# Kernel tuning notes

Hardware: AMD Instinct MI355X
Metric: run time of the kernel (lower is better)

The kernel has to match this reference:

```python
import jax, jax.numpy as jnp
import numpy as np

HEADS, OUT_CH = 8, 32  # GATConv(128, 256//8, heads=8) -> concat width 256
NEG_SLOPE = 0.2


def setup_inputs() -> dict:
    key = jax.random.key(0)
    ks = jax.random.split(key, 12)
    N, E, F_IN = 50000, 500000, 128
    H, C = HEADS, OUT_CH
    HID = H * C            # 256
    x = jax.random.normal(ks[0], (N, F_IN), dtype=jnp.float32)
    edge_index = jax.random.randint(ks[1], (2, E), 0, N, dtype=jnp.int64)
    s = 1.0 / np.sqrt(F_IN)
    W_gat = jax.random.normal(ks[2], (F_IN, H * C), dtype=jnp.float32) * s
    att_src = jax.random.normal(ks[3], (H, C), dtype=jnp.float32) * (1.0 / np.sqrt(C))
    att_dst = jax.random.normal(ks[4], (H, C), dtype=jnp.float32) * (1.0 / np.sqrt(C))
    b_gat = jnp.zeros((HID,), dtype=jnp.float32)
    W1 = jax.random.normal(ks[5], (HID, HID // 2), dtype=jnp.float32) * (1.0 / np.sqrt(HID))
    b1 = jnp.zeros((HID // 2,), dtype=jnp.float32)
    W2 = jax.random.normal(ks[6], (HID // 2, 6), dtype=jnp.float32) * (1.0 / np.sqrt(HID // 2))
    b2 = jnp.zeros((6,), dtype=jnp.float32)
    return {"x": x, "edge_index": edge_index, "W_gat": W_gat, "att_src": att_src,
            "att_dst": att_dst, "b_gat": b_gat, "W1": W1, "b1": b1, "W2": W2, "b2": b2}


def _gat_forward(x, edge_index, W_gat, att_src, att_dst, b_gat):
    N = x.shape[0]
    H, C = HEADS, OUT_CH
    # add self loops (PyG GATConv default)
    loop = jnp.arange(N, dtype=edge_index.dtype)
    src = jnp.concatenate([edge_index[0], loop])
    dst = jnp.concatenate([edge_index[1], loop])
    # per-node transform: [N, H, C]
    xh = (x @ W_gat).reshape(N, H, C)
    a_src = jnp.einsum('nhc,hc->nh', xh, att_src)  # [N, H]
    a_dst = jnp.einsum('nhc,hc->nh', xh, att_dst)  # [N, H]
    alpha = a_src[src] + a_dst[dst]                # [Etot, H]
    alpha = jnp.where(alpha >= 0, alpha, NEG_SLOPE * alpha)  # leaky relu
    # segment softmax over destination nodes
    m = jax.ops.segment_max(alpha, dst, num_segments=N)     # [N, H]
    m = jax.lax.stop_gradient(m)
    ex = jnp.exp(alpha - m[dst])
    denom = jax.ops.segment_sum(ex, dst, num_segments=N)    # [N, H]
    coef = ex / denom[dst]                                   # [Etot, H]
    # weighted scatter-add aggregation
    msgs = xh[src] * coef[:, :, None]                        # [Etot, H, C]
    out = jax.ops.segment_sum(msgs, dst, num_segments=N)     # [N, H, C]
    return out.reshape(N, H * C) + b_gat


def reference(x, edge_index, W_gat, att_src, att_dst, b_gat, W1, b1, W2, b2):
    h = _gat_forward(x, edge_index, W_gat, att_src, att_dst, b_gat)
    h = jax.nn.elu(h)
    g = jnp.mean(h, axis=0, keepdims=True)   # [1, 256] mean pool
    g = jax.nn.relu(g @ W1 + b1)
    return g @ W2 + b2                        # [1, 6] logits
```

## Files before the change

### kernel.cpp

```cpp
#include <hip/hip_runtime.h>
#include <hip/hip_fp8.h>
#include <math.h>

#define F_IN 128
#define HID 256
#define NH 8
#define CAP 40
#define BCAP 4096
#define AGG_BLOCKS 768

typedef _Float16 h16;
typedef __attribute__((ext_vector_type(8))) _Float16 half8;
typedef __attribute__((ext_vector_type(4))) float f32x4;

__device__ inline unsigned char f32_to_fp8(float v) {
#if __has_builtin(__builtin_amdgcn_cvt_pk_fp8_f32)
    return (unsigned char)(__builtin_amdgcn_cvt_pk_fp8_f32(v, v, 0, false) & 0xff);
#else
    __hip_fp8_e4m3 t(v);
    return (unsigned char)t.__x;
#endif
}

__device__ inline void fp8x4_to_f32(int w, float* out) {
#if __has_builtin(__builtin_amdgcn_cvt_pk_f32_fp8)
    auto lo = __builtin_amdgcn_cvt_pk_f32_fp8(w, false);
    auto hi = __builtin_amdgcn_cvt_pk_f32_fp8(w, true);
    out[0] = lo[0]; out[1] = lo[1]; out[2] = hi[0]; out[3] = hi[1];
#else
    #pragma unroll
    for (int k = 0; k < 4; ++k) {
        __hip_fp8_e4m3 t;
        t.__x = (unsigned char)((w >> (8 * k)) & 0xff);
        out[k] = (float)t;
    }
#endif
}

__global__ void k_prep(const float* __restrict__ Wg,
                       const float* __restrict__ att_s,
                       const float* __restrict__ att_d,
                       h16* __restrict__ Wt_sw,
                       int* gcur, float* g2, int n) {
    int i = blockIdx.x * 256 + threadIdx.x;
    if (i < 256) gcur[i] = 0;
    if (i < 256 * HID) g2[i] = 0.f;
    if (i < 4352) {
        int fid = i;
        int lane16 = fid & 15;
        int quad = (fid >> 4) & 3;
        int ks = (fid >> 6) & 3;
        int ct = fid >> 8;
        int k0 = ks * 32 + quad * 8;
        half8 v;
        if (ct < 16) {
            int col = ct * 16 + lane16;
            #pragma unroll
            for (int j = 0; j < 8; ++j) v[j] = (h16)Wg[(size_t)(k0 + j) * HID + col];
        } else {
            const float* att = (lane16 < 8) ? att_s : att_d;
            int h = lane16 & 7;
            #pragma unroll
            for (int j = 0; j < 8; ++j) {
                float s = 0.f;
                for (int c = 0; c < 32; ++c)
                    s += Wg[(size_t)(k0 + j) * HID + h * 32 + c] * att[h * 32 + c];
                v[j] = (h16)s;
            }
        }
        *(half8*)(Wt_sw + (size_t)fid * 8) = v;
    }
}

__global__ __launch_bounds__(512) void k_ga(const float* __restrict__ x,
                                            const h16* __restrict__ Wt_sw,
                                            const int* __restrict__ dstp,
                                            const int* __restrict__ srcp,
                                            unsigned char* __restrict__ xh8,
                                            float* __restrict__ a_src,
                                            float* __restrict__ a_dst,
                                            unsigned int* __restrict__ gbuck,
                                            int* __restrict__ gcur,
                                            int n, int e, int ntiles,
                                            int nbuck, int npart) {
    __shared__ __align__(16) char smem[65536];
    int t = threadIdx.x;

    if (blockIdx.x < (unsigned)npart) {
        int* hist  = (int*)smem;
        int* scn   = hist + 256;
        int* lbase = scn + 256;
        int* lcur  = lbase + 256;
        int* base  = lcur + 256;
        unsigned int* sorted = (unsigned int*)(base + 256);
        int c0 = blockIdx.x * 4096;

        if (t < 256) hist[t] = 0;
        __syncthreads();

        unsigned int w8[8];
        int b8[8];
        #pragma unroll
        for (int k = 0; k < 8; ++k) {
            int i = c0 + k * 512 + t;
            if (i < e) {
                int d = dstp[i];
                int s = srcp[i];
                int b = d >> 8;
                b8[k] = b;
                w8[k] = ((unsigned)b << 24) | ((unsigned)(d & 255) << 16) | (unsigned)s;
                atomicAdd(&hist[b], 1);
            } else {
                b8[k] = -1;
                w8[k] = 0;
            }
        }
        __syncthreads();
        if (t < 256) scn[t] = hist[t];
        __syncthreads();
        for (int off = 1; off < 256; off <<= 1) {
            int u = 0;
            if (t < 256 && t >= off) u = scn[t - off];
            __syncthreads();
            if (t < 256 && t >= off) scn[t] += u;
            __syncthreads();
        }
        if (t < 256) {
            lbase[t] = scn[t] - hist[t];
            lcur[t] = 0;
            if (t < nbuck && hist[t] > 0) base[t] = atomicAdd(&gcur[t], hist[t]);
        }
        __syncthreads();
        #pragma unroll
        for (int k = 0; k < 8; ++k) {
            if (b8[k] >= 0) {
                int r = atomicAdd(&lcur[b8[k]], 1);
                sorted[lbase[b8[k]] + r] = w8[k];
            }
        }
        __syncthreads();
        int total = scn[255];
        for (int j = t; j < total; j += 512) {
            unsigned int w = sorted[j];
            int b = w >> 24;
            int addr = base[b] + (j - lbase[b]);
            if (addr < BCAP) gbuck[(size_t)b * BCAP + addr] = w;
        }
        return;
    }

    h16* wlds = (h16*)smem;
    int w = t >> 6, l = t & 63;
    int lane16 = l & 15, quad = l >> 4;

    float4 pv0[4], pv1[4];
    half8 bA[4];
    int tile = (blockIdx.x - npart) * 8 + w;
    bool have = tile < ntiles;
    int row0 = tile * 16;
    {
        const half8* wq = (const half8*)Wt_sw;
        #pragma unroll
        for (int ks = 0; ks < 4; ++ks) bA[ks] = wq[(64 + ks) * 64 + l];
    }
    if (have) {
        int rA = row0 + lane16;
        if (rA >= n) rA = n - 1;
        const float* xrow = x + (size_t)rA * F_IN + quad * 8;
        #pragma unroll
        for (int ks = 0; ks < 4; ++ks) {
            pv0[ks] = *(const float4*)(xrow + ks * 32);
            pv1[ks] = *(const float4*)(xrow + ks * 32 + 4);
        }
    }
    {
        const int4* wsrc = (const int4*)Wt_sw;
        int4* wdst = (int4*)wlds;
        #pragma unroll
        for (int i = 0; i < 8; ++i) wdst[i * 512 + t] = wsrc[i * 512 + t];
    }
    __syncthreads();
    if (!have) return;
    const h16* wl = wlds + (size_t)l * 8;

    half8 afr[4];
    #pragma unroll
    for (int ks = 0; ks < 4; ++ks) {
        half8 a;
        a[0] = (h16)pv0[ks].x; a[1] = (h16)pv0[ks].y;
        a[2] = (h16)pv0[ks].z; a[3] = (h16)pv0[ks].w;
        a[4] = (h16)pv1[ks].x; a[5] = (h16)pv1[ks].y;
        a[6] = (h16)pv1[ks].z; a[7] = (h16)pv1[ks].w;
        afr[ks] = a;
    }
    f32x4 acc[16];
    #pragma unroll
    for (int ct = 0; ct < 16; ++ct) acc[ct] = (f32x4){0.f, 0.f, 0.f, 0.f};
    #pragma unroll
    for (int ct = 0; ct < 16; ++ct) {
        #pragma unroll
        for (int ks = 0; ks < 4; ++ks) {
            half8 bfr = *(const half8*)(wl + (ct * 4 + ks) * 512);
            acc[ct] = __builtin_amdgcn_mfma_f32_16x16x32_f16(afr[ks], bfr, acc[ct], 0, 0, 0);
        }
    }
    f32x4 acc16 = (f32x4){0.f, 0.f, 0.f, 0.f};
    #pragma unroll
    for (int ks = 0; ks < 4; ++ks)
        acc16 = __builtin_amdgcn_mfma_f32_16x16x32_f16(afr[ks], bA[ks], acc16, 0, 0, 0);

    if (row0 + 16 <= n) {
        #pragma unroll
        for (int ct = 0; ct < 16; ++ct) {
            int col = ct * 16 + lane16;
            #pragma unroll
            for (int r = 0; r < 4; ++r)
                xh8[(size_t)(row0 + quad * 4 + r) * HID + col] = f32_to_fp8(acc[ct][r]);
        }
        float* ap = (lane16 < 8) ? a_src : a_dst;
        int h = lane16 & 7;
        #pragma unroll
        for (int r = 0; r < 4; ++r)
            ap[(row0 + quad * 4 + r) * NH + h] = acc16[r];
    } else {
        #pragma unroll
        for (int ct = 0; ct < 16; ++ct) {
            int col = ct * 16 + lane16;
            #pragma unroll
            for (int r = 0; r < 4; ++r) {
                int row = row0 + quad * 4 + r;
                if (row < n) xh8[(size_t)row * HID + col] = f32_to_fp8(acc[ct][r]);
            }
        }
        float* ap = (lane16 < 8) ? a_src : a_dst;
        int h = lane16 & 7;
        #pragma unroll
        for (int r = 0; r < 4; ++r) {
            int row = row0 + quad * 4 + r;
            if (row < n) ap[row * NH + h] = acc16[r];
        }
    }
}

__global__ __launch_bounds__(256) void k_bin(const unsigned int* __restrict__ gbuck,
                                             const int* __restrict__ gcur,
                                             int* __restrict__ cnt,
                                             unsigned short* __restrict__ bin,
                                             int n, int nbuck) {
    __shared__ int hist[256];
    __shared__ int cur[256];
    __shared__ __align__(16) unsigned short bl[256 * CAP];
    int t = threadIdx.x;
    int b = blockIdx.x;
    int count = gcur[b];
    if (count > BCAP) count = BCAP;
    hist[t] = 0;
    __syncthreads();
    const unsigned int* bb = gbuck + (size_t)b * BCAP;
    for (int j = t; j < count; j += 256) atomicAdd(&hist[(bb[j] >> 16) & 255], 1);
    __syncthreads();
    int node = b * 256 + t;
    if (node < n) {
        int hh = hist[t];
        cnt[node] = hh > CAP ? CAP : hh;
    }
    cur[t] = 0;
    __syncthreads();
    for (int j = t; j < count; j += 256) {
        unsigned int wv = bb[j];
        int dl = (wv >> 16) & 255;
        int pos = atomicAdd(&cur[dl], 1);
        if (pos < CAP) bl[dl * CAP + pos] = (unsigned short)(wv & 0xffff);
    }
    __syncthreads();
    const int4* s4 = (const int4*)bl;
    int4* d4 = (int4*)(bin + (size_t)b * 256 * CAP);
    #pragma unroll
    for (int q = 0; q < 5; ++q) d4[q * 256 + t] = s4[q * 256 + t];
}

__global__ __launch_bounds__(256) void k_agg(const unsigned char* __restrict__ xh8,
                                             const float* __restrict__ a_src,
                                             const float* __restrict__ a_dst,
                                             const int* __restrict__ cnt,
                                             const unsigned short* __restrict__ bin,
                                             const float* __restrict__ b_gat,
                                             float* __restrict__ g2, int n, int ntl) {
    __shared__ float wpart[4][260];
    int t = threadIdx.x;
    int slot = t >> 4;
    int cl = t & 15;
    int c0 = cl * 16;
    int h = cl >> 1;

    float vacc[16];
    #pragma unroll
    for (int i = 0; i < 16; ++i) vacc[i] = 0.f;

    for (int tile = blockIdx.x; tile < ntl; tile += gridDim.x) {
        int nn = tile * 16 + slot;
        bool alive = nn < n;
        int nnc = alive ? nn : (n - 1);

        float ad = a_dst[nnc * NH + h];
        int deg = cnt[nnc];
        if (deg > CAP) deg = CAP;

        float al = a_src[nnc * NH + h] + ad;
        al = al > 0.f ? al : 0.2f * al;
        float ex = __expf(al);
        float den = ex;
        float acc[16];
        {
            int4 v = *(const int4*)(xh8 + (size_t)nnc * HID + c0);
            float f[16];
            fp8x4_to_f32(v.x, f); fp8x4_to_f32(v.y, f + 4);
            fp8x4_to_f32(v.z, f + 8); fp8x4_to_f32(v.w, f + 12);
            #pragma unroll
            for (int i = 0; i < 16; ++i) acc[i] = ex * f[i];
        }
        const unsigned short* brow = bin + (size_t)nnc * CAP;
        int j = 0;
        for (; j + 4 <= deg; j += 4) {
            ushort4 ss = *(const ushort4*)(brow + j);
            int s0 = ss.x, s1 = ss.y, s2 = ss.z, s3 = ss.w;
            float aa[4];
            aa[0] = a_src[s0 * NH + h];
            aa[1] = a_src[s1 * NH + h];
            aa[2] = a_src[s2 * NH + h];
            aa[3] = a_src[s3 * NH + h];
            int4 v0 = *(const int4*)(xh8 + (size_t)s0 * HID + c0);
            int4 v1 = *(const int4*)(xh8 + (size_t)s1 * HID + c0);
            int4 v2 = *(const int4*)(xh8 + (size_t)s2 * HID + c0);
            int4 v3 = *(const int4*)(xh8 + (size_t)s3 * HID + c0);
            float e4[4];
            #pragma unroll
            for (int q = 0; q < 4; ++q) {
                float a2 = aa[q] + ad;
                a2 = a2 > 0.f ? a2 : 0.2f * a2;
                e4[q] = __expf(a2);
                den += e4[q];
            }
            float f[16];
            fp8x4_to_f32(v0.x, f); fp8x4_to_f32(v0.y, f + 4);
            fp8x4_to_f32(v0.z, f + 8); fp8x4_to_f32(v0.w, f + 12);
            #pragma unroll
            for (int i = 0; i < 16; ++i) acc[i] += e4[0] * f[i];
            fp8x4_to_f32(v1.x, f); fp8x4_to_f32(v1.y, f + 4);
            fp8x4_to_f32(v1.z, f + 8); fp8x4_to_f32(v1.w, f + 12);
            #pragma unroll
            for (int i = 0; i < 16; ++i) acc[i] += e4[1] * f[i];
            fp8x4_to_f32(v2.x, f); fp8x4_to_f32(v2.y, f + 4);
            fp8x4_to_f32(v2.z, f + 8); fp8x4_to_f32(v2.w, f + 12);
            #pragma unroll
            for (int i = 0; i < 16; ++i) acc[i] += e4[2] * f[i];
            fp8x4_to_f32(v3.x, f); fp8x4_to_f32(v3.y, f + 4);
            fp8x4_to_f32(v3.z, f + 8); fp8x4_to_f32(v3.w, f + 12);
            #pragma unroll
            for (int i = 0; i < 16; ++i) acc[i] += e4[3] * f[i];
        }
        for (; j < deg; ++j) {
            int s = brow[j];
            float a2 = a_src[s * NH + h] + ad;
            a2 = a2 > 0.f ? a2 : 0.2f * a2;
            float e2 = __expf(a2);
            den += e2;
            int4 v = *(const int4*)(xh8 + (size_t)s * HID + c0);
            float f[16];
            fp8x4_to_f32(v.x, f); fp8x4_to_f32(v.y, f + 4);
            fp8x4_to_f32(v.z, f + 8); fp8x4_to_f32(v.w, f + 12);
            #pragma unroll
            for (int i = 0; i < 16; ++i) acc[i] += e2 * f[i];
        }
        float inv = 1.f / den;
        #pragma unroll
        for (int q = 0; q < 4; ++q) {
            float4 bv = *(const float4*)(b_gat + c0 + q * 4);
            float v0 = acc[q * 4 + 0] * inv + bv.x;
            float v1 = acc[q * 4 + 1] * inv + bv.y;
            float v2 = acc[q * 4 + 2] * inv + bv.z;
            float v3 = acc[q * 4 + 3] * inv + bv.w;
            v0 = v0 > 0.f ? v0 : expm1f(v0);
            v1 = v1 > 0.f ? v1 : expm1f(v1);
            v2 = v2 > 0.f ? v2 : expm1f(v2);
            v3 = v3 > 0.f ? v3 : expm1f(v3);
            if (alive) {
                vacc[q * 4 + 0] += v0;
                vacc[q * 4 + 1] += v1;
                vacc[q * 4 + 2] += v2;
                vacc[q * 4 + 3] += v3;
            }
        }
    }
    #pragma unroll
    for (int i = 0; i < 16; ++i) {
        vacc[i] += __shfl_xor(vacc[i], 16, 64);
        vacc[i] += __shfl_xor(vacc[i], 32, 64);
    }
    int w = t >> 6, lw = t & 63;
    if (lw < 16) {
        #pragma unroll
        for (int q = 0; q < 4; ++q)
            *(f32x4*)(&wpart[w][c0 + q * 4]) =
                (f32x4){vacc[q * 4], vacc[q * 4 + 1], vacc[q * 4 + 2], vacc[q * 4 + 3]};
    }
    __syncthreads();
    float s = wpart[0][t] + wpart[1][t] + wpart[2][t] + wpart[3][t];
    atomicAdd(&g2[(blockIdx.x & 255) * HID + t], s);
}

__global__ __launch_bounds__(256) void k_mlp(const float* __restrict__ g2,
                                             const float* __restrict__ W1,
                                             const float* __restrict__ b1,
                                             const float* __restrict__ W2,
                                             const float* __restrict__ b2,
                                             float* __restrict__ out, int n) {
    __shared__ float gm[HID];
    __shared__ float h1p[2][128];
    __shared__ float h1[128];
    int t = threadIdx.x;
    float s = 0.f;
    for (int b = 0; b < 256; ++b) s += g2[b * HID + t];
    gm[t] = s / (float)n;
    __syncthreads();
    int o = t & 127, hf = t >> 7;
    float a = 0.f;
    #pragma unroll 4
    for (int k = hf * 128; k < hf * 128 + 128; ++k) a += gm[k] * W1[k * 128 + o];
    h1p[hf][o] = a;
    __syncthreads();
    if (t < 128) {
        float v = h1p[0][t] + h1p[1][t] + b1[t];
        h1[t] = v > 0.f ? v : 0.f;
    }
    __syncthreads();
    if (t < 6) {
        float a2 = b2[t];
        for (int k = 0; k < 128; ++k) a2 += h1[k] * W2[k * 6 + t];
        out[t] = a2;
    }
}

extern "C" void kernel_launch(void* const* d_in, const int* in_sizes, int n_in,
                              void* d_out, int out_size, void* d_ws, size_t ws_size,
                              hipStream_t stream) {
    const float* x     = (const float*)d_in[0];
    const int*   ei    = (const int*)d_in[1];
    const float* Wg    = (const float*)d_in[2];
    const float* att_s = (const float*)d_in[3];
    const float* att_d = (const float*)d_in[4];
    const float* b_gat = (const float*)d_in[5];
    const float* W1    = (const float*)d_in[6];
    const float* b1    = (const float*)d_in[7];
    const float* W2    = (const float*)d_in[8];
    const float* b2    = (const float*)d_in[9];

    int N = in_sizes[0] / F_IN;
    int E = in_sizes[1] / 2;
    const int* srcp = ei;
    const int* dstp = ei + E;
    int nblk = (N + 15) / 16;
    int ntiles = (N + 15) / 16;
    int nbuck = (N + 255) >> 8;

    char* ws = (char*)d_ws;
    size_t off = 0;
    auto alloc = [&](size_t bytes) {
        size_t o = off;
        off += (bytes + 255) & ~(size_t)255;
        return o;
    };
    unsigned char* xh8 = (unsigned char*)(ws + alloc((size_t)N * HID));
    h16*   Wt      = (h16*)(ws + alloc((size_t)4352 * 16));
    float* asr     = (float*)(ws + alloc((size_t)N * NH * 4));
    float* ads     = (float*)(ws + alloc((size_t)N * NH * 4));
    int*   cnt     = (int*)(ws + alloc((size_t)N * 4));
    unsigned short* bin = (unsigned short*)(ws + alloc((size_t)nbuck * 256 * CAP * 2));
    float* g2      = (float*)(ws + alloc((size_t)256 * HID * 4));
    unsigned int* gbuck = (unsigned int*)(ws + alloc((size_t)nbuck * BCAP * 4));
    int*   gcur    = (int*)(ws + alloc((size_t)256 * 4));

    int npart = (E + 4095) / 4096;
    int ngemm = (ntiles + 7) / 8;
    int naggb = nblk < AGG_BLOCKS ? nblk : AGG_BLOCKS;

    k_prep<<<256, 256, 0, stream>>>(Wg, att_s, att_d, Wt, gcur, g2, N);
    k_ga<<<npart + ngemm, 512, 0, stream>>>(x, Wt, dstp, srcp,
                                            xh8, asr, ads, gbuck, gcur,
                                            N, E, ntiles, nbuck, npart);
    k_bin<<<nbuck, 256, 0, stream>>>(gbuck, gcur, cnt, bin, N, nbuck);
    k_agg<<<naggb, 256, 0, stream>>>(xh8, asr, ads, cnt, bin, b_gat, g2, N, nblk);
    k_mlp<<<1, 256, 0, stream>>>(g2, W1, b1, W2, b2, (float*)d_out, N);
}
```

Measured before the change: 181.7 us.

## Fuse binning, aggregation and MLP into one kernel with last-block finalize

Merges the bucket-binning, attention aggregation and MLP head into a single kernel. Each block takes a quarter of a bucket, builds its neighbor lists in shared memory, aggregates its 64 nodes, then the last block to finish (tracked by an atomic counter) runs the MLP. This removes two kernel launches and the global cnt/bin round trip, and shrinks the partial-sum buffer. The cost is that each bucket's edge list is scanned four times, and the grid is fixed at about 4 blocks per bucket instead of a persistent grid.

After: 233.3 us. 1.28x slower.

```diff
diff --git a/kernel.cpp b/kernel.cpp
--- a/kernel.cpp
+++ b/kernel.cpp
@@ -7,7 +7,7 @@
 #define NH 8
 #define CAP 40
 #define BCAP 4096
-#define AGG_BLOCKS 768
+#define G2R 64
 
 typedef _Float16 h16;
 typedef __attribute__((ext_vector_type(8))) _Float16 half8;
@@ -41,10 +41,10 @@
                        const float* __restrict__ att_s,
                        const float* __restrict__ att_d,
                        h16* __restrict__ Wt_sw,
-                       int* gcur, float* g2, int n) {
+                       int* gcur, float* g2r, int n) {
     int i = blockIdx.x * 256 + threadIdx.x;
-    if (i < 256) gcur[i] = 0;
-    if (i < 256 * HID) g2[i] = 0.f;
+    if (i < 260) gcur[i] = 0;
+    if (i < G2R * HID) g2r[i] = 0.f;
     if (i < 4352) {
         int fid = i;
         int lane16 = fid & 15;
@@ -242,52 +242,49 @@
     }
 }
 
-__global__ __launch_bounds__(256) void k_bin(const unsigned int* __restrict__ gbuck,
-                                             const int* __restrict__ gcur,
-                                             int* __restrict__ cnt,
-                                             unsigned short* __restrict__ bin,
-                                             int n, int nbuck) {
-    __shared__ int hist[256];
-    __shared__ int cur[256];
-    __shared__ __align__(16) unsigned short bl[256 * CAP];
+__global__ __launch_bounds__(256) void k_aggm(const unsigned char* __restrict__ xh8,
+                                              const float* __restrict__ a_src,
+                                              const float* __restrict__ a_dst,
+                                              const unsigned int* __restrict__ gbuck,
+                                              const int* __restrict__ gcur,
+                                              const float* __restrict__ b_gat,
+                                              float* __restrict__ g2r,
+                                              int* __restrict__ done,
+                                              const float* __restrict__ W1,
+                                              const float* __restrict__ b1,
+                                              const float* __restrict__ W2,
+                                              const float* __restrict__ b2,
+                                              float* __restrict__ out, int n) {
+    __shared__ int hist[64];
+    __shared__ int cur[64];
+    __shared__ __align__(16) unsigned short bl[64 * CAP];
+    __shared__ float wpart[4][260];
+    __shared__ int amlast;
     int t = threadIdx.x;
-    int b = blockIdx.x;
-    int count = gcur[b];
+    int bucket = blockIdx.x >> 2;
+    int q = blockIdx.x & 3;
+    int node0 = bucket * 256 + q * 64;
+
+    int count = gcur[bucket];
     if (count > BCAP) count = BCAP;
-    hist[t] = 0;
-    __syncthreads();
-    const unsigned int* bb = gbuck + (size_t)b * BCAP;
-    for (int j = t; j < count; j += 256) atomicAdd(&hist[(bb[j] >> 16) & 255], 1);
-    __syncthreads();
-    int node = b * 256 + t;
-    if (node < n) {
-        int hh = hist[t];
-        cnt[node] = hh > CAP ? CAP : hh;
-    }
-    cur[t] = 0;
+    if (t < 64) { hist[t] = 0; cur[t] = 0; }
+    __syncthreads();
+    const unsigned int* bb = gbuck + (size_t)bucket * BCAP;
+    for (int j = t; j < count; j += 256) {
+        int dl = (bb[j] >> 16) & 255;
+        if ((dl >> 6) == q) atomicAdd(&hist[dl & 63], 1);
+    }
     __syncthreads();
     for (int j = t; j < count; j += 256) {
         unsigned int wv = bb[j];
         int dl = (wv >> 16) & 255;
-        int pos = atomicAdd(&cur[dl], 1);
-        if (pos < CAP) bl[dl * CAP + pos] = (unsigned short)(wv & 0xffff);
-    }
-    __syncthreads();
-    const int4* s4 = (const int4*)bl;
-    int4* d4 = (int4*)(bin + (size_t)b * 256 * CAP);
-    #pragma unroll
-    for (int q = 0; q < 5; ++q) d4[q * 256 + t] = s4[q * 256 + t];
-}
-
-__global__ __launch_bounds__(256) void k_agg(const unsigned char* __restrict__ xh8,
-                                             const float* __restrict__ a_src,
-                                             const float* __restrict__ a_dst,
-                                             const int* __restrict__ cnt,
-                                             const unsigned short* __restrict__ bin,
-                                             const float* __restrict__ b_gat,
-                                             float* __restrict__ g2, int n, int ntl) {
-    __shared__ float wpart[4][260];
-    int t = threadIdx.x;
+        if ((dl >> 6) == q) {
+            int pos = atomicAdd(&cur[dl & 63], 1);
+            if (pos < CAP) bl[(dl & 63) * CAP + pos] = (unsigned short)(wv & 0xffff);
+        }
+    }
+    __syncthreads();
+
     int slot = t >> 4;
     int cl = t & 15;
     int c0 = cl * 16;
@@ -297,13 +294,14 @@
     #pragma unroll
     for (int i = 0; i < 16; ++i) vacc[i] = 0.f;
 
-    for (int tile = blockIdx.x; tile < ntl; tile += gridDim.x) {
-        int nn = tile * 16 + slot;
+    for (int it = 0; it < 4; ++it) {
+        int lidx = it * 16 + slot;
+        int nn = node0 + lidx;
         bool alive = nn < n;
         int nnc = alive ? nn : (n - 1);
 
         float ad = a_dst[nnc * NH + h];
-        int deg = cnt[nnc];
+        int deg = alive ? hist[lidx] : 0;
         if (deg > CAP) deg = CAP;
 
         float al = a_src[nnc * NH + h] + ad;
@@ -319,7 +317,7 @@
             #pragma unroll
             for (int i = 0; i < 16; ++i) acc[i] = ex * f[i];
         }
-        const unsigned short* brow = bin + (size_t)nnc * CAP;
+        const unsigned short* brow = bl + lidx * CAP;
         int j = 0;
         for (; j + 4 <= deg; j += 4) {
             ushort4 ss = *(const ushort4*)(brow + j);
@@ -335,11 +333,11 @@
             int4 v3 = *(const int4*)(xh8 + (size_t)s3 * HID + c0);
             float e4[4];
             #pragma unroll
-            for (int q = 0; q < 4; ++q) {
-                float a2 = aa[q] + ad;
+            for (int qq = 0; qq < 4; ++qq) {
+                float a2 = aa[qq] + ad;
                 a2 = a2 > 0.f ? a2 : 0.2f * a2;
-                e4[q] = __expf(a2);
-                den += e4[q];
+                e4[qq] = __expf(a2);
+                den += e4[qq];
             }
             float f[16];
             fp8x4_to_f32(v0.x, f); fp8x4_to_f32(v0.y, f + 4);
@@ -374,21 +372,21 @@
         }
         float inv = 1.f / den;
         #pragma unroll
-        for (int q = 0; q < 4; ++q) {
-            float4 bv = *(const float4*)(b_gat + c0 + q * 4);
-            float v0 = acc[q * 4 + 0] * inv + bv.x;
-            float v1 = acc[q * 4 + 1] * inv + bv.y;
-            float v2 = acc[q * 4 + 2] * inv + bv.z;
-            float v3 = acc[q * 4 + 3] * inv + bv.w;
+        for (int qq = 0; qq < 4; ++qq) {
+            float4 bv = *(const float4*)(b_gat + c0 + qq * 4);
+            float v0 = acc[qq * 4 + 0] * inv + bv.x;
+            float v1 = acc[qq * 4 + 1] * inv + bv.y;
+            float v2 = acc[qq * 4 + 2] * inv + bv.z;
+            float v3 = acc[qq * 4 + 3] * inv + bv.w;
             v0 = v0 > 0.f ? v0 : expm1f(v0);
             v1 = v1 > 0.f ? v1 : expm1f(v1);
             v2 = v2 > 0.f ? v2 : expm1f(v2);
             v3 = v3 > 0.f ? v3 : expm1f(v3);
             if (alive) {
-                vacc[q * 4 + 0] += v0;
-                vacc[q * 4 + 1] += v1;
-                vacc[q * 4 + 2] += v2;
-                vacc[q * 4 + 3] += v3;
+                vacc[qq * 4 + 0] += v0;
+                vacc[qq * 4 + 1] += v1;
+                vacc[qq * 4 + 2] += v2;
+                vacc[qq * 4 + 3] += v3;
             }
         }
     }
@@ -400,28 +398,27 @@
     int w = t >> 6, lw = t & 63;
     if (lw < 16) {
         #pragma unroll
-        for (int q = 0; q < 4; ++q)
-            *(f32x4*)(&wpart[w][c0 + q * 4]) =
-                (f32x4){vacc[q * 4], vacc[q * 4 + 1], vacc[q * 4 + 2], vacc[q * 4 + 3]};
+        for (int qq = 0; qq < 4; ++qq)
+            *(f32x4*)(&wpart[w][c0 + qq * 4]) =
+                (f32x4){vacc[qq * 4], vacc[qq * 4 + 1], vacc[qq * 4 + 2], vacc[qq * 4 + 3]};
     }
     __syncthreads();
     float s = wpart[0][t] + wpart[1][t] + wpart[2][t] + wpart[3][t];
-    atomicAdd(&g2[(blockIdx.x & 255) * HID + t], s);
-}
-
-__global__ __launch_bounds__(256) void k_mlp(const float* __restrict__ g2,
-                                             const float* __restrict__ W1,
-                                             const float* __restrict__ b1,
-                                             const float* __restrict__ W2,
-                                             const float* __restrict__ b2,
-                                             float* __restrict__ out, int n) {
+    atomicAdd(&g2r[(blockIdx.x & (G2R - 1)) * HID + t], s);
+
+    __threadfence();
+    __syncthreads();
+    if (t == 0) amlast = (atomicAdd(done, 1) == (int)gridDim.x - 1) ? 1 : 0;
+    __syncthreads();
+    if (!amlast) return;
+
     __shared__ float gm[HID];
     __shared__ float h1p[2][128];
     __shared__ float h1[128];
-    int t = threadIdx.x;
-    float s = 0.f;
-    for (int b = 0; b < 256; ++b) s += g2[b * HID + t];
-    gm[t] = s / (float)n;
+    float s2 = 0.f;
+    for (int r = 0; r < G2R; ++r)
+        s2 += __hip_atomic_load(&g2r[r * HID + t], __ATOMIC_RELAXED, __HIP_MEMORY_SCOPE_AGENT);
+    gm[t] = s2 / (float)n;
     __syncthreads();
     int o = t & 127, hf = t >> 7;
     float a = 0.f;
@@ -459,7 +456,6 @@
     int E = in_sizes[1] / 2;
     const int* srcp = ei;
     const int* dstp = ei + E;
-    int nblk = (N + 15) / 16;
     int ntiles = (N + 15) / 16;
     int nbuck = (N + 255) >> 8;
 
@@ -474,21 +470,19 @@
     h16*   Wt      = (h16*)(ws + alloc((size_t)4352 * 16));
     float* asr     = (float*)(ws + alloc((size_t)N * NH * 4));
     float* ads     = (float*)(ws + alloc((size_t)N * NH * 4));
-    int*   cnt     = (int*)(ws + alloc((size_t)N * 4));
-    unsigned short* bin = (unsigned short*)(ws + alloc((size_t)nbuck * 256 * CAP * 2));
-    float* g2      = (float*)(ws + alloc((size_t)256 * HID * 4));
+    float* g2r     = (float*)(ws + alloc((size_t)G2R * HID * 4));
     unsigned int* gbuck = (unsigned int*)(ws + alloc((size_t)nbuck * BCAP * 4));
-    int*   gcur    = (int*)(ws + alloc((size_t)256 * 4));
+    int*   gcur    = (int*)(ws + alloc((size_t)512 * 4));
+    int*   done    = gcur + 256;
 
     int npart = (E + 4095) / 4096;
     int ngemm = (ntiles + 7) / 8;
-    int naggb = nblk < AGG_BLOCKS ? nblk : AGG_BLOCKS;
-
-    k_prep<<<256, 256, 0, stream>>>(Wg, att_s, att_d, Wt, gcur, g2, N);
+
+    k_prep<<<256, 256, 0, stream>>>(Wg, att_s, att_d, Wt, gcur, g2r, N);
     k_ga<<<npart + ngemm, 512, 0, stream>>>(x, Wt, dstp, srcp,
                                             xh8, asr, ads, gbuck, gcur,
                                             N, E, ntiles, nbuck, npart);
-    k_bin<<<nbuck, 256, 0, stream>>>(gbuck, gcur, cnt, bin, N, nbuck);
-    k_agg<<<naggb, 256, 0, stream>>>(xh8, asr, ads, cnt, bin, b_gat, g2, N, nblk);
-    k_mlp<<<1, 256, 0, stream>>>(g2, W1, b1, W2, b2, (float*)d_out, N);
-}
+    k_aggm<<<4 * nbuck, 256, 0, stream>>>(xh8, asr, ads, gbuck, gcur, b_gat,
+                                          g2r, done, W1, b1, W2, b2,
+                                          (float*)d_out, N);
+}
```

## Fuse MLP into aggregation via last-block pattern, one tile per block, smaller partitions

Applied to the files above, without the earlier changes.

Folds the final MLP kernel into the aggregation kernel: each block bumps a done counter, and the last block to finish reads the partial sums with atomic loads and runs the MLP. This removes one launch. Aggregation now launches one block per 16-node tile instead of a grid-stride loop over a capped grid. Edge partitioning chunks shrink from 4096 to 2048 edges per block, which doubles the number of partition blocks. The trade-offs are extra block scheduling overhead, a serialized tail in the last block, and more global atomics on the bucket counters.

New measurement: 383.3 us. 111% more time.

```diff
diff --git a/kernel.cpp b/kernel.cpp
--- a/kernel.cpp
+++ b/kernel.cpp
@@ -7,7 +7,6 @@
 #define NH 8
 #define CAP 40
 #define BCAP 4096
-#define AGG_BLOCKS 768
 
 typedef _Float16 h16;
 typedef __attribute__((ext_vector_type(8))) _Float16 half8;
@@ -43,7 +42,7 @@
                        h16* __restrict__ Wt_sw,
                        int* gcur, float* g2, int n) {
     int i = blockIdx.x * 256 + threadIdx.x;
-    if (i < 256) gcur[i] = 0;
+    if (i < 260) gcur[i] = 0;
     if (i < 256 * HID) g2[i] = 0.f;
     if (i < 4352) {
         int fid = i;
@@ -93,26 +92,26 @@
         int* lcur  = lbase + 256;
         int* base  = lcur + 256;
         unsigned int* sorted = (unsigned int*)(base + 256);
-        int c0 = blockIdx.x * 4096;
+        int c0 = blockIdx.x * 2048;
 
         if (t < 256) hist[t] = 0;
         __syncthreads();
 
-        unsigned int w8[8];
-        int b8[8];
-        #pragma unroll
-        for (int k = 0; k < 8; ++k) {
+        unsigned int w4[4];
+        int b4[4];
+        #pragma unroll
+        for (int k = 0; k < 4; ++k) {
             int i = c0 + k * 512 + t;
             if (i < e) {
                 int d = dstp[i];
                 int s = srcp[i];
                 int b = d >> 8;
-                b8[k] = b;
-                w8[k] = ((unsigned)b << 24) | ((unsigned)(d & 255) << 16) | (unsigned)s;
+                b4[k] = b;
+                w4[k] = ((unsigned)b << 24) | ((unsigned)(d & 255) << 16) | (unsigned)s;
                 atomicAdd(&hist[b], 1);
             } else {
-                b8[k] = -1;
-                w8[k] = 0;
+                b4[k] = -1;
+                w4[k] = 0;
             }
         }
         __syncthreads();
@@ -132,10 +131,10 @@
         }
         __syncthreads();
         #pragma unroll
-        for (int k = 0; k < 8; ++k) {
-            if (b8[k] >= 0) {
-                int r = atomicAdd(&lcur[b8[k]], 1);
-                sorted[lbase[b8[k]] + r] = w8[k];
+        for (int k = 0; k < 4; ++k) {
+            if (b4[k] >= 0) {
+                int r = atomicAdd(&lcur[b4[k]], 1);
+                sorted[lbase[b4[k]] + r] = w4[k];
             }
         }
         __syncthreads();
@@ -285,143 +284,139 @@
                                              const int* __restrict__ cnt,
                                              const unsigned short* __restrict__ bin,
                                              const float* __restrict__ b_gat,
-                                             float* __restrict__ g2, int n, int ntl) {
+                                             float* __restrict__ g2,
+                                             int* __restrict__ done,
+                                             const float* __restrict__ W1,
+                                             const float* __restrict__ b1,
+                                             const float* __restrict__ W2,
+                                             const float* __restrict__ b2,
+                                             float* __restrict__ out, int n) {
     __shared__ float wpart[4][260];
+    __shared__ int amlast;
     int t = threadIdx.x;
     int slot = t >> 4;
     int cl = t & 15;
     int c0 = cl * 16;
     int h = cl >> 1;
-
-    float vacc[16];
-    #pragma unroll
-    for (int i = 0; i < 16; ++i) vacc[i] = 0.f;
-
-    for (int tile = blockIdx.x; tile < ntl; tile += gridDim.x) {
-        int nn = tile * 16 + slot;
-        bool alive = nn < n;
-        int nnc = alive ? nn : (n - 1);
-
-        float ad = a_dst[nnc * NH + h];
-        int deg = cnt[nnc];
-        if (deg > CAP) deg = CAP;
-
-        float al = a_src[nnc * NH + h] + ad;
-        al = al > 0.f ? al : 0.2f * al;
-        float ex = __expf(al);
-        float den = ex;
-        float acc[16];
-        {
-            int4 v = *(const int4*)(xh8 + (size_t)nnc * HID + c0);
-            float f[16];
-            fp8x4_to_f32(v.x, f); fp8x4_to_f32(v.y, f + 4);
-            fp8x4_to_f32(v.z, f + 8); fp8x4_to_f32(v.w, f + 12);
-            #pragma unroll
-            for (int i = 0; i < 16; ++i) acc[i] = ex * f[i];
-        }
-        const unsigned short* brow = bin + (size_t)nnc * CAP;
-        int j = 0;
-        for (; j + 4 <= deg; j += 4) {
-            ushort4 ss = *(const ushort4*)(brow + j);
-            int s0 = ss.x, s1 = ss.y, s2 = ss.z, s3 = ss.w;
-            float aa[4];
-            aa[0] = a_src[s0 * NH + h];
-            aa[1] = a_src[s1 * NH + h];
-            aa[2] = a_src[s2 * NH + h];
-            aa[3] = a_src[s3 * NH + h];
-            int4 v0 = *(const int4*)(xh8 + (size_t)s0 * HID + c0);
-            int4 v1 = *(const int4*)(xh8 + (size_t)s1 * HID + c0);
-            int4 v2 = *(const int4*)(xh8 + (size_t)s2 * HID + c0);
-            int4 v3 = *(const int4*)(xh8 + (size_t)s3 * HID + c0);
-            float e4[4];
-            #pragma unroll
-            for (int q = 0; q < 4; ++q) {
-                float a2 = aa[q] + ad;
-                a2 = a2 > 0.f ? a2 : 0.2f * a2;
-                e4[q] = __expf(a2);
-                den += e4[q];
-            }
-            float f[16];
-            fp8x4_to_f32(v0.x, f); fp8x4_to_f32(v0.y, f + 4);
-            fp8x4_to_f32(v0.z, f + 8); fp8x4_to_f32(v0.w, f + 12);
-            #pragma unroll
-            for (int i = 0; i < 16; ++i) acc[i] += e4[0] * f[i];
-            fp8x4_to_f32(v1.x, f); fp8x4_to_f32(v1.y, f + 4);
-            fp8x4_to_f32(v1.z, f + 8); fp8x4_to_f32(v1.w, f + 12);
-            #pragma unroll
-            for (int i = 0; i < 16; ++i) acc[i] += e4[1] * f[i];
-            fp8x4_to_f32(v2.x, f); fp8x4_to_f32(v2.y, f + 4);
-            fp8x4_to_f32(v2.z, f + 8); fp8x4_to_f32(v2.w, f + 12);
-            #pragma unroll
-            for (int i = 0; i < 16; ++i) acc[i] += e4[2] * f[i];
-            fp8x4_to_f32(v3.x, f); fp8x4_to_f32(v3.y, f + 4);
-            fp8x4_to_f32(v3.z, f + 8); fp8x4_to_f32(v3.w, f + 12);
-            #pragma unroll
-            for (int i = 0; i < 16; ++i) acc[i] += e4[3] * f[i];
-        }
-        for (; j < deg; ++j) {
-            int s = brow[j];
-            float a2 = a_src[s * NH + h] + ad;
+    int nn = blockIdx.x * 16 + slot;
+    bool alive = nn < n;
+    int nnc = alive ? nn : (n - 1);
+
+    float ad = a_dst[nnc * NH + h];
+    int deg = cnt[nnc];
+    if (deg > CAP) deg = CAP;
+
+    float al = a_src[nnc * NH + h] + ad;
+    al = al > 0.f ? al : 0.2f * al;
+    float ex = __expf(al);
+    float den = ex;
+    float acc[16];
+    {
+        int4 v = *(const int4*)(xh8 + (size_t)nnc * HID + c0);
+        float f[16];
+        fp8x4_to_f32(v.x, f); fp8x4_to_f32(v.y, f + 4);
+        fp8x4_to_f32(v.z, f + 8); fp8x4_to_f32(v.w, f + 12);
+        #pragma unroll
+        for (int i = 0; i < 16; ++i) acc[i] = ex * f[i];
+    }
+    const unsigned short* brow = bin + (size_t)nnc * CAP;
+    int j = 0;
+    for (; j + 4 <= deg; j += 4) {
+        ushort4 ss = *(const ushort4*)(brow + j);
+        int s0 = ss.x, s1 = ss.y, s2 = ss.z, s3 = ss.w;
+        float aa[4];
+        aa[0] = a_src[s0 * NH + h];
+        aa[1] = a_src[s1 * NH + h];
+        aa[2] = a_src[s2 * NH + h];
+        aa[3] = a_src[s3 * NH + h];
+        int4 v0 = *(const int4*)(xh8 + (size_t)s0 * HID + c0);
+        int4 v1 = *(const int4*)(xh8 + (size_t)s1 * HID + c0);
+        int4 v2 = *(const int4*)(xh8 + (size_t)s2 * HID + c0);
+        int4 v3 = *(const int4*)(xh8 + (size_t)s3 * HID + c0);
+        float e4[4];
+        #pragma unroll
+        for (int q = 0; q < 4; ++q) {
+            float a2 = aa[q] + ad;
             a2 = a2 > 0.f ? a2 : 0.2f * a2;
-            float e2 = __expf(a2);
-            den += e2;
-            int4 v = *(const int4*)(xh8 + (size_t)s * HID + c0);
-            float f[16];
-            fp8x4_to_f32(v.x, f); fp8x4_to_f32(v.y, f + 4);
-            fp8x4_to_f32(v.z, f + 8); fp8x4_to_f32(v.w, f + 12);
-            #pragma unroll
-            for (int i = 0; i < 16; ++i) acc[i] += e2 * f[i];
-        }
-        float inv = 1.f / den;
-        #pragma unroll
-        for (int q = 0; q < 4; ++q) {
-            float4 bv = *(const float4*)(b_gat + c0 + q * 4);
-            float v0 = acc[q * 4 + 0] * inv + bv.x;
-            float v1 = acc[q * 4 + 1] * inv + bv.y;
-            float v2 = acc[q * 4 + 2] * inv + bv.z;
-            float v3 = acc[q * 4 + 3] * inv + bv.w;
-            v0 = v0 > 0.f ? v0 : expm1f(v0);
-            v1 = v1 > 0.f ? v1 : expm1f(v1);
-            v2 = v2 > 0.f ? v2 : expm1f(v2);
-            v3 = v3 > 0.f ? v3 : expm1f(v3);
-            if (alive) {
-                vacc[q * 4 + 0] += v0;
-                vacc[q * 4 + 1] += v1;
-                vacc[q * 4 + 2] += v2;
-                vacc[q * 4 + 3] += v3;
-            }
-        }
+            e4[q] = __expf(a2);
+            den += e4[q];
+        }
+        float f[16];
+        fp8x4_to_f32(v0.x, f); fp8x4_to_f32(v0.y, f + 4);
+        fp8x4_to_f32(v0.z, f + 8); fp8x4_to_f32(v0.w, f + 12);
+        #pragma unroll
+        for (int i = 0; i < 16; ++i) acc[i] += e4[0] * f[i];
+        fp8x4_to_f32(v1.x, f); fp8x4_to_f32(v1.y, f + 4);
+        fp8x4_to_f32(v1.z, f + 8); fp8x4_to_f32(v1.w, f + 12);
+        #pragma unroll
+        for (int i = 0; i < 16; ++i) acc[i] += e4[1] * f[i];
+        fp8x4_to_f32(v2.x, f); fp8x4_to_f32(v2.y, f + 4);
+        fp8x4_to_f32(v2.z, f + 8); fp8x4_to_f32(v2.w, f + 12);
+        #pragma unroll
+        for (int i = 0; i < 16; ++i) acc[i] += e4[2] * f[i];
+        fp8x4_to_f32(v3.x, f); fp8x4_to_f32(v3.y, f + 4);
+        fp8x4_to_f32(v3.z, f + 8); fp8x4_to_f32(v3.w, f + 12);
+        #pragma unroll
+        for (int i = 0; i < 16; ++i) acc[i] += e4[3] * f[i];
+    }
+    for (; j < deg; ++j) {
+        int s = brow[j];
+        float a2 = a_src[s * NH + h] + ad;
+        a2 = a2 > 0.f ? a2 : 0.2f * a2;
+        float e2 = __expf(a2);
+        den += e2;
+        int4 v = *(const int4*)(xh8 + (size_t)s * HID + c0);
+        float f[16];
+        fp8x4_to_f32(v.x, f); fp8x4_to_f32(v.y, f + 4);
+        fp8x4_to_f32(v.z, f + 8); fp8x4_to_f32(v.w, f + 12);
+        #pragma unroll
+        for (int i = 0; i < 16; ++i) acc[i] += e2 * f[i];
+    }
+    float inv = 1.f / den;
+    float val[16];
+    #pragma unroll
+    for (int q = 0; q < 4; ++q) {
+        float4 bv = *(const float4*)(b_gat + c0 + q * 4);
+        val[q * 4 + 0] = acc[q * 4 + 0] * inv + bv.x;
+        val[q * 4 + 1] = acc[q * 4 + 1] * inv + bv.y;
+        val[q * 4 + 2] = acc[q * 4 + 2] * inv + bv.z;
+        val[q * 4 + 3] = acc[q * 4 + 3] * inv + bv.w;
     }
     #pragma unroll
     for (int i = 0; i < 16; ++i) {
-        vacc[i] += __shfl_xor(vacc[i], 16, 64);
-        vacc[i] += __shfl_xor(vacc[i], 32, 64);
+        float v = val[i];
+        v = v > 0.f ? v : expm1f(v);
+        val[i] = alive ? v : 0.f;
+    }
+    #pragma unroll
+    for (int i = 0; i < 16; ++i) {
+        val[i] += __shfl_xor(val[i], 16, 64);
+        val[i] += __shfl_xor(val[i], 32, 64);
     }
     int w = t >> 6, lw = t & 63;
     if (lw < 16) {
         #pragma unroll
         for (int q = 0; q < 4; ++q)
             *(f32x4*)(&wpart[w][c0 + q * 4]) =
-                (f32x4){vacc[q * 4], vacc[q * 4 + 1], vacc[q * 4 + 2], vacc[q * 4 + 3]};
+                (f32x4){val[q * 4], val[q * 4 + 1], val[q * 4 + 2], val[q * 4 + 3]};
     }
     __syncthreads();
     float s = wpart[0][t] + wpart[1][t] + wpart[2][t] + wpart[3][t];
     atomicAdd(&g2[(blockIdx.x & 255) * HID + t], s);
-}
-
-__global__ __launch_bounds__(256) void k_mlp(const float* __restrict__ g2,
-                                             const float* __restrict__ W1,
-                                             const float* __restrict__ b1,
-                                             const float* __restrict__ W2,
-                                             const float* __restrict__ b2,
-                                             float* __restrict__ out, int n) {
+
+    __threadfence();
+    __syncthreads();
+    if (t == 0) amlast = (atomicAdd(done, 1) == (int)gridDim.x - 1) ? 1 : 0;
+    __syncthreads();
+    if (!amlast) return;
+
     __shared__ float gm[HID];
     __shared__ float h1p[2][128];
     __shared__ float h1[128];
-    int t = threadIdx.x;
-    float s = 0.f;
-    for (int b = 0; b < 256; ++b) s += g2[b * HID + t];
-    gm[t] = s / (float)n;
+    float s2 = 0.f;
+    for (int r = 0; r < 256; ++r)
+        s2 += __hip_atomic_load(&g2[r * HID + t], __ATOMIC_RELAXED, __HIP_MEMORY_SCOPE_AGENT);
+    gm[t] = s2 / (float)n;
     __syncthreads();
     int o = t & 127, hf = t >> 7;
     float a = 0.f;
@@ -478,17 +473,17 @@
     unsigned short* bin = (unsigned short*)(ws + alloc((size_t)nbuck * 256 * CAP * 2));
     float* g2      = (float*)(ws + alloc((size_t)256 * HID * 4));
     unsigned int* gbuck = (unsigned int*)(ws + alloc((size_t)nbuck * BCAP * 4));
-    int*   gcur    = (int*)(ws + alloc((size_t)256 * 4));
-
-    int npart = (E + 4095) / 4096;
+    int*   gcur    = (int*)(ws + alloc((size_t)512 * 4));
+    int*   done    = gcur + 256;
+
+    int npart = (E + 2047) / 2048;
     int ngemm = (ntiles + 7) / 8;
-    int naggb = nblk < AGG_BLOCKS ? nblk : AGG_BLOCKS;
 
     k_prep<<<256, 256, 0, stream>>>(Wg, att_s, att_d, Wt, gcur, g2, N);
     k_ga<<<npart + ngemm, 512, 0, stream>>>(x, Wt, dstp, srcp,
                                             xh8, asr, ads, gbuck, gcur,
                                             N, E, ntiles, nbuck, npart);
     k_bin<<<nbuck, 256, 0, stream>>>(gbuck, gcur, cnt, bin, N, nbuck);
-    k_agg<<<naggb, 256, 0, stream>>>(xh8, asr, ads, cnt, bin, b_gat, g2, N, nblk);
-    k_mlp<<<1, 256, 0, stream>>>(g2, W1, b1, W2, b2, (float*)d_out, N);
-}
+    k_agg<<<nblk, 256, 0, stream>>>(xh8, asr, ads, cnt, bin, b_gat, g2, done,
+                                    W1, b1, W2, b2, (float*)d_out, N);
+}
```
